# Kernel optimization log

Measured on AMD Instinct MI355X. Metric: run time of the kernel, lower is better.

## Reference

```python
import jax, jax.numpy as jnp
import numpy as np

B, L, SIZE, HEADS, AH, NBR, KER, DEPTH = 64, 512, 128, 8, 16, 15, 16, 3
MAXD = 20.0
N = B * L
EDGE = KER + 3 + 9 + 1  # 29


def _normalize(v):
    return v / (jnp.linalg.norm(v, axis=-1, keepdims=True) + 1e-8)


def _frames(pos):
    # local orientation frame per residue from consecutive CA displacements
    u = _normalize(pos[1:] - pos[:-1])            # (N-1,3)
    up = jnp.concatenate([u[:1], u], axis=0)      # u_{i-1}
    un = jnp.concatenate([u, u[-1:]], axis=0)     # u_i
    b = _normalize(up - un)
    n = _normalize(jnp.cross(up, un))
    return jnp.stack([b, n, jnp.cross(b, n)], axis=-1)  # (N,3,3)


def setup_inputs() -> dict:
    key = jax.random.key(0)
    ks = jax.random.split(key, 16)
    g = lambda i, shape, s=1.0: jax.random.normal(ks[i], shape, jnp.float32) * s
    return {
        "tertiary": g(0, (N, 3, 3), 10.0),
        "sequence": g(1, (N, 20)),
        "subgraph_indices": jnp.arange(N, dtype=jnp.int32) // L,
        "knn_noise": g(2, (B, L, L)),
        "embed_w": g(3, (27, SIZE), 0.1), "embed_b": jnp.zeros((SIZE,), jnp.float32),
        "wq": g(4, (DEPTH, SIZE, HEADS * AH), 0.08),
        "wk": g(5, (DEPTH, SIZE + EDGE, HEADS * AH), 0.08),
        "wv": g(6, (DEPTH, SIZE + EDGE, HEADS * AH), 0.08),
        "wo": g(7, (DEPTH, HEADS * AH, SIZE), 0.08),
        "mlp_w1": g(8, (DEPTH, SIZE, SIZE), 0.08), "mlp_b1": jnp.zeros((DEPTH, SIZE), jnp.float32),
        "mlp_w2": g(9, (DEPTH, SIZE, SIZE), 0.08), "mlp_b2": jnp.zeros((DEPTH, SIZE), jnp.float32),
        "mlp_w3": g(10, (DEPTH, SIZE, SIZE), 0.08), "mlp_b3": jnp.zeros((DEPTH, SIZE), jnp.float32),
        "pool_w": g(11, (4, SIZE, SIZE, 3), 0.05), "pool_b": jnp.zeros((4, SIZE), jnp.float32),
        "energy_w": g(12, (SIZE, 1), 0.1), "energy_b": jnp.zeros((1,), jnp.float32),
    }


def _forward(tertiary, sequence, knn_noise, embed_w, embed_b, wq, wk, wv, wo,
             mlp_w1, mlp_b1, mlp_w2, mlp_b2, mlp_w3, mlp_b3,
             pool_w, pool_b, energy_w, energy_b):
    pos = tertiary[:, 1]                                   # (N,3) CA positions
    R = _frames(pos)                                       # (N,3,3)
    # ---- kNN per contiguous protein group with noisy distances ----
    pg = pos.reshape(B, L, 3)
    dist = jnp.linalg.norm(pg[:, :, None] - pg[:, None, :], axis=-1)  # (B,L,L)
    closeness = -dist + 3.0 * knn_noise
    idx = jax.lax.top_k(closeness, NBR)[1]                 # (B,L,NBR) local
    nbr = (idx + (jnp.arange(B) * L)[:, None, None]).reshape(N, NBR)
    # ---- RBF relative encoding (RelativeStructure.message) ----
    dvec = pos[nbr] - pos[:, None]                         # (N,NBR,3)
    d = jnp.linalg.norm(dvec, axis=-1)                     # (N,NBR)
    mu = jnp.linspace(0.0, MAXD, KER)
    sigma = MAXD / KER
    rbf = jnp.exp(-(((d[..., None] - mu) / sigma) ** 2))   # (N,NBR,KER)
    dirs = jnp.einsum('nrc,nkr->nkc', R, dvec / (d[..., None] + 1e-8))
    relrot = jnp.einsum('nrc,nkrd->nkcd', R, R[nbr]).reshape(N, NBR, 9)
    ind = jnp.arange(N, dtype=tertiary.dtype)
    relind = (ind[nbr] - ind[:, None])[..., None]
    edge = jnp.concatenate([rbf, dirs, relrot, relind], axis=-1)  # (N,NBR,EDGE)
    # ---- structured graph-attention encoder ----
    h = jnp.ones((N, 27), tertiary.dtype) @ embed_w + embed_b
    inv_sqrt = 1.0 / np.sqrt(AH).astype(np.float32)
    for l in range(DEPTH):
        q = (h @ wq[l]).reshape(N, HEADS, AH)
        kv = jnp.concatenate([h[nbr], edge], axis=-1)      # (N,NBR,SIZE+EDGE)
        k = (kv @ wk[l]).reshape(N, NBR, HEADS, AH)
        v = (kv @ wv[l]).reshape(N, NBR, HEADS, AH)
        logits = jnp.einsum('nhd,nkhd->nhk', q, k) * inv_sqrt
        a = jax.nn.softmax(logits, axis=-1)
        o = jnp.einsum('nhk,nkhd->nhd', a, v).reshape(N, HEADS * AH) @ wo[l]
        h = h + o
        m = jax.nn.relu(h @ mlp_w1[l] + mlp_b1[l])
        m = jax.nn.relu(m @ mlp_w2[l] + mlp_b2[l])
        h = h + m @ mlp_w3[l] + mlp_b3[l]
    # ---- scatter-pad pool: residual conv + maxpool(2), x4, then length-sum ----
    x = h.reshape(B, L, SIZE).transpose(0, 2, 1)           # (B,SIZE,L)
    for i in range(4):
        y = jax.lax.conv_general_dilated(
            x, pool_w[i], (1,), ((1, 1),),
            dimension_numbers=('NCH', 'OIH', 'NCH')) + pool_b[i][None, :, None]
        x = x + jax.nn.leaky_relu(y, 0.01)
        Lc = x.shape[-1]
        x = x.reshape(B, SIZE, Lc // 2, 2).max(axis=-1)
    pooled = x.sum(axis=-1)                                # (B,SIZE)
    return pooled @ energy_w + energy_b                    # (B,1)


def reference(tertiary, sequence, subgraph_indices, knn_noise, embed_w, embed_b,
              wq, wk, wv, wo, mlp_w1, mlp_b1, mlp_w2, mlp_b2, mlp_w3, mlp_b3,
              pool_w, pool_b, energy_w, energy_b):
    # subgraph_indices encodes contiguous equal-size groups (arange // L)
    return _forward(tertiary, sequence, knn_noise, embed_w, embed_b, wq, wk, wv, wo,
                    mlp_w1, mlp_b1, mlp_w2, mlp_b2, mlp_w3, mlp_b3,
                    pool_w, pool_b, energy_w, energy_b)
```

## Files before the change

kernel.cpp:

```cpp
#include <hip/hip_runtime.h>
#include <math.h>

#define N_TOT 32768
#define NNBR 15
#define APW 8
#define ELPH 40
#define ETP 20
#define PLP 20

#define KNB 4096
#define FRB 128
#define PRB 3392

typedef __attribute__((ext_vector_type(8))) _Float16 f16x8;
typedef __attribute__((ext_vector_type(2))) _Float16 f16x2;
typedef __attribute__((ext_vector_type(4))) float f32x4;

#define CBAR() __asm__ volatile("" ::: "memory")
#define PAIR(v, c) __builtin_shufflevector(v, v, 2 * (c), 2 * (c) + 1)

__device__ __forceinline__ _Float16 f2h(float x) { return (_Float16)x; }

__device__ __forceinline__ float fdot2(f16x2 a, f16x2 b, float c) {
  float d;
  asm("v_dot2_f32_f16 %0, %1, %2, %3" : "=v"(d) : "v"(a), "v"(b), "v"(c));
  return d;
}

template <int CTRL>
__device__ __forceinline__ float dpp_mov_f32(float x) {
  return __int_as_float(
      __builtin_amdgcn_update_dpp(0, __float_as_int(x), CTRL, 0xf, 0xf, true));
}

template <int CTRL>
__device__ __forceinline__ unsigned dpp_max_u32(unsigned x) {
  unsigned y = (unsigned)__builtin_amdgcn_update_dpp(0, (int)x, CTRL, 0xf, 0xf, true);
  return y > x ? y : x;
}

template <int CTRL>
__device__ __forceinline__ unsigned long long dpp_max_u64(unsigned long long x) {
  unsigned lo = (unsigned)__builtin_amdgcn_update_dpp(
      0, (int)(unsigned)x, CTRL, 0xf, 0xf, true);
  unsigned hi = (unsigned)__builtin_amdgcn_update_dpp(
      0, (int)(unsigned)(x >> 32), CTRL, 0xf, 0xf, true);
  unsigned long long y = ((unsigned long long)hi << 32) | lo;
  return y > x ? y : x;
}

__device__ __forceinline__ void ins3v(unsigned s, int j,
                                      unsigned& m1v, int& i1,
                                      unsigned& m2v, int& i2,
                                      unsigned& m3v, int& i3) {
  bool g1 = s > m1v;
  unsigned t = g1 ? m1v : s;  int it = g1 ? i1 : j;
  m1v = g1 ? s : m1v;         i1  = g1 ? j  : i1;
  bool g2 = t > m2v;
  unsigned u = g2 ? m2v : t;  int iu = g2 ? i2 : it;
  m2v = g2 ? t : m2v;         i2  = g2 ? it : i2;
  bool g3 = u > m3v;
  m3v = g3 ? u : m3v;         i3  = g3 ? iu : i3;
}

__global__ __launch_bounds__(256) void k_pre(
    const float* __restrict__ tert, const float* __restrict__ noise,
    int* __restrict__ nbr, float* __restrict__ pos, float* __restrict__ R,
    const float* __restrict__ wq, const float* __restrict__ wk,
    const float* __restrict__ wv, const float* __restrict__ wo,
    const float* __restrict__ w1, const float* __restrict__ w2,
    const float* __restrict__ w3, _Float16* __restrict__ wbt,
    _Float16* __restrict__ wqk, _Float16* __restrict__ wpe,
    const float* __restrict__ pw, _Float16* __restrict__ wct,
    const float* __restrict__ ew, const float* __restrict__ ebias,
    _Float16* __restrict__ h) {
  __shared__ float posL[512 * 3];
  __shared__ float hvS[128];
  int bb = blockIdx.x, tid = threadIdx.x;
  if (bb < KNB) {
    int b = bb >> 6;
    int n0 = b << 9;
    for (int i = tid; i < 1536; i += 256) {
      int r = i / 3, c = i - r * 3;
      posL[i] = tert[(size_t)(n0 + r) * 9 + 3 + c];
    }
    __syncthreads();
    int wave = tid >> 6, lane = tid & 63;
    int l = lane & 31;
    int rloc = (bb & 63) * 8 + wave * 2 + (lane >> 5);
    int row = n0 + rloc;
    const float* nrow = noise + (size_t)row * 512;
    float pix = posL[rloc * 3 + 0];
    float piy = posL[rloc * 3 + 1];
    float piz = posL[rloc * 3 + 2];
    unsigned m1v = 0u, m2v = 0u, m3v = 0u;
    int i1 = 0, i2 = 0, i3 = 0;
#pragma unroll
    for (int jj = 0; jj < 16; jj++) {
      int j = l + jj * 32;
      float dx = posL[j * 3 + 0] - pix;
      float dy = posL[j * 3 + 1] - piy;
      float dz = posL[j * 3 + 2] - piz;
      float c = -sqrtf(dx * dx + dy * dy + dz * dz) + 3.f * nrow[j];
      unsigned u = __float_as_uint(c);
      unsigned s = u ^ (unsigned)(((int)u >> 31) | (int)0x80000000);
      ins3v(s, j, m1v, i1, m2v, i2, m3v, i3);
    }
    int jmine = 0;
#pragma unroll 1
    for (int it = 0; it < NNBR; it++) {
      unsigned r = m1v;
      r = dpp_max_u32<0x111>(r);
      r = dpp_max_u32<0x112>(r);
      r = dpp_max_u32<0x114>(r);
      r = dpp_max_u32<0x118>(r);
      r = dpp_max_u32<0x142>(r);
      unsigned gA = (unsigned)__builtin_amdgcn_readlane((int)r, 31);
      unsigned gB = (unsigned)__builtin_amdgcn_readlane((int)r, 63);
      unsigned gsel = (lane & 32) ? gB : gA;
      bool match = (m1v == gsel);
      unsigned long long mk = __ballot((int)match);
      unsigned mA = (unsigned)mk, mB = (unsigned)(mk >> 32);
      int jA = __builtin_amdgcn_readlane(i1, __ffs(mA) - 1);
      int jB = __builtin_amdgcn_readlane(i1, 31 + __ffs(mB));
      if (__popc(mA) > 1 || __popc(mB) > 1) {
        unsigned long long pk = ((unsigned long long)m1v << 9) | (unsigned)(511 - i1);
        pk = dpp_max_u64<0x111>(pk);
        pk = dpp_max_u64<0x112>(pk);
        pk = dpp_max_u64<0x114>(pk);
        pk = dpp_max_u64<0x118>(pk);
        pk = dpp_max_u64<0x142>(pk);
        unsigned pA = (unsigned)__builtin_amdgcn_readlane((int)(unsigned)pk, 31);
        unsigned pB = (unsigned)__builtin_amdgcn_readlane((int)(unsigned)pk, 63);
        if (__popc(mA) > 1) jA = 511 - (int)(pA & 511u);
        if (__popc(mB) > 1) jB = 511 - (int)(pB & 511u);
      }
      int j = (lane & 32) ? jB : jA;
      if (l == it) jmine = j;
      bool win = match && (i1 == j);
      if (win) { m1v = m2v; i1 = i2; m2v = m3v; i2 = i3; m3v = 0u; }
      if (__any((int)(win && m1v == 0u))) {
        if (win && m1v == 0u) {
          unsigned gv = gsel; int gj = j;
          unsigned a1 = 0u, a2 = 0u, a3 = 0u;
          int b1i = 0, b2i = 0, b3i = 0;
#pragma unroll 1
          for (int jj = 0; jj < 16; jj++) {
            int j2 = l + jj * 32;
            float dx = posL[j2 * 3 + 0] - pix;
            float dy = posL[j2 * 3 + 1] - piy;
            float dz = posL[j2 * 3 + 2] - piz;
            float c = -sqrtf(dx * dx + dy * dy + dz * dz) + 3.f * nrow[j2];
            unsigned u = __float_as_uint(c);
            unsigned s = u ^ (unsigned)(((int)u >> 31) | (int)0x80000000);
            bool keep = (s < gv) || (s == gv && j2 > gj);
            ins3v(keep ? s : 0u, j2, a1, b1i, a2, b2i, a3, b3i);
          }
          m1v = a1; i1 = b1i; m2v = a2; i2 = b2i; m3v = a3; i3 = b3i;
        }
      }
    }
    if (l < NNBR) nbr[(size_t)row * NNBR + l] = n0 + jmine;
  } else if (bb < KNB + FRB) {
    int n = (bb - KNB) * 256 + tid;
    if (n >= N_TOT) return;
    float px = tert[n * 9 + 3], py = tert[n * 9 + 4], pz = tert[n * 9 + 5];
    pos[n * 3 + 0] = px; pos[n * 3 + 1] = py; pos[n * 3 + 2] = pz;
    int i0 = (n > 0) ? (n - 1) : 0;
    int i1 = (n < N_TOT - 1) ? n : (N_TOT - 2);
    float ax = tert[(i0 + 1) * 9 + 3] - tert[i0 * 9 + 3];
    float ay = tert[(i0 + 1) * 9 + 4] - tert[i0 * 9 + 4];
    float az = tert[(i0 + 1) * 9 + 5] - tert[i0 * 9 + 5];
    float il = 1.f / (sqrtf(ax * ax + ay * ay + az * az) + 1e-8f);
    float ux = ax * il, uy = ay * il, uz = az * il;
    float cx = tert[(i1 + 1) * 9 + 3] - tert[i1 * 9 + 3];
    float cy = tert[(i1 + 1) * 9 + 4] - tert[i1 * 9 + 4];
    float cz = tert[(i1 + 1) * 9 + 5] - tert[i1 * 9 + 5];
    il = 1.f / (sqrtf(cx * cx + cy * cy + cz * cz) + 1e-8f);
    float vx = cx * il, vy = cy * il, vz = cz * il;
    float bx = ux - vx, by = uy - vy, bz = uz - vz;
    il = 1.f / (sqrtf(bx * bx + by * by + bz * bz) + 1e-8f);
    bx *= il; by *= il; bz *= il;
    float nx = uy * vz - uz * vy;
    float ny = uz * vx - ux * vz;
    float nz = ux * vy - uy * vx;
    il = 1.f / (sqrtf(nx * nx + ny * ny + nz * nz) + 1e-8f);
    nx *= il; ny *= il; nz *= il;
    float ex = by * nz - bz * ny;
    float ey = bz * nx - bx * nz;
    float ez = bx * ny - by * nx;
    float* Rn = R + (size_t)n * 9;
    Rn[0] = bx; Rn[1] = nx; Rn[2] = ex;
    Rn[3] = by; Rn[4] = ny; Rn[5] = ey;
    Rn[6] = bz; Rn[7] = nz; Rn[8] = ez;
  } else {
    int pb2 = bb - (KNB + FRB);
    if (pb2 < 1344) {
      int idx = pb2 * 256 + tid;
      int lL = idx / (7 * 16384);
      int r = idx % (7 * 16384);
      int w = r / 16384;
      int e = r % 16384;
      int k = e >> 7, n = e & 127;
      float val;
      switch (w) {
        case 0: val = wq[(size_t)lL * 16384 + e]; break;
        case 1: val = wk[(size_t)lL * 157 * 128 + e]; break;
        case 2: val = wv[(size_t)lL * 157 * 128 + e]; break;
        case 3: val = wo[(size_t)lL * 16384 + e]; break;
        case 4: val = w1[(size_t)lL * 16384 + e]; break;
        case 5: val = w2[(size_t)lL * 16384 + e]; break;
        default: val = w3[(size_t)lL * 16384 + e]; break;
      }
      wbt[(size_t)(lL * 7 + w) * 16384 + n * 128 + k] = f2h(val);
    } else if (pb2 < 1728) {
      int idx = (pb2 - 1344) * 256 + tid;
      int lL = idx / 32768;
      int r = idx % 32768;
      int blk = r >> 14;
      int jp = (r >> 7) & 127;
      int c = r & 127;
      int j = blk * 128 + jp;
      int hh = j >> 5, e = j & 31;
      float val = 0.f;
      if (e < 29) {
        const float* wqp = wq + (size_t)lL * 16384 + (size_t)c * 128 + hh * 16;
        const float* wkp = wk + (size_t)lL * 157 * 128 + (size_t)(128 + e) * 128 + hh * 16;
        float s = 0.f;
#pragma unroll
        for (int d = 0; d < 16; d++) s = fmaf(wqp[d], wkp[d], s);
        val = 0.25f * s;
      }
      wqk[(size_t)idx] = f2h(val);
    } else if (pb2 < 2112) {
      int idx = (pb2 - 1728) * 256 + tid;
      int lL = idx / 32768;
      int r = idx % 32768;
      int blk = r >> 14;
      int cout = (r >> 7) & 127;
      int jp = r & 127;
      int j = blk * 128 + jp;
      float val = 0.f;
      if (j < 232) {
        int e = j >> 3, hh = j & 7;
        const float* wvp = wv + (size_t)lL * 157 * 128 + (size_t)(128 + e) * 128 + hh * 16;
        const float* wop = wo + (size_t)lL * 16384 + (size_t)(hh * 16) * 128 + cout;
#pragma unroll
        for (int d = 0; d < 16; d++) val = fmaf(wvp[d], wop[d * 128], val);
      }
      wpe[(size_t)idx] = f2h(val);
    } else if (pb2 < 2880) {
      int idx = (pb2 - 2112) * 256 + tid;
      int kt = idx % 3;
      int rest = idx / 3;
      int i = rest % 128; rest /= 128;
      int oo = rest % 128;
      int s = rest / 128;
      wct[(((size_t)s * 3 + kt) * 128 + oo) * 128 + i] = f2h(pw[idx]);
    } else {
      int vb = pb2 - 2880;
      if (tid < 128) {
        float s = ebias[tid];
#pragma unroll
        for (int i = 0; i < 27; i++) s += ew[i * 128 + tid];
        hvS[tid] = s;
      }
      __syncthreads();
      size_t total = (size_t)N_TOT * 128;
      for (size_t j = (size_t)vb * 256 + tid; j < total; j += (size_t)512 * 256)
        h[j] = f2h(hvS[j & 127]);
    }
  }
}

__global__ __launch_bounds__(256) void k_edge(const float* __restrict__ pos,
                                              const float* __restrict__ R,
                                              const int* __restrict__ nbr,
                                              _Float16* __restrict__ edge) {
  int idx = blockIdx.x * 256 + threadIdx.x;
  if (idx >= N_TOT * NNBR) return;
  int n = idx / NNBR;
  int m = nbr[idx];
  float dx = pos[m * 3 + 0] - pos[n * 3 + 0];
  float dy = pos[m * 3 + 1] - pos[n * 3 + 1];
  float dz = pos[m * 3 + 2] - pos[n * 3 + 2];
  float d = sqrtf(dx * dx + dy * dy + dz * dz);
  _Float16 eb[32];
#pragma unroll
  for (int j = 0; j < 16; j++) {
    float mu = (20.f / 15.f) * (float)j;
    float t = (d - mu) * 0.8f;
    eb[j] = f2h(__expf(-t * t));
  }
  float inv = 1.f / (d + 1e-8f);
  float ux = dx * inv, uy = dy * inv, uz = dz * inv;
  float Rn[9], Rm[9];
#pragma unroll
  for (int j = 0; j < 9; j++) { Rn[j] = R[(size_t)n * 9 + j]; Rm[j] = R[(size_t)m * 9 + j]; }
#pragma unroll
  for (int cc = 0; cc < 3; cc++)
    eb[16 + cc] = f2h(Rn[0 * 3 + cc] * ux + Rn[1 * 3 + cc] * uy + Rn[2 * 3 + cc] * uz);
#pragma unroll
  for (int cc = 0; cc < 3; cc++)
#pragma unroll
    for (int dd = 0; dd < 3; dd++)
      eb[19 + cc * 3 + dd] = f2h(Rn[0 * 3 + cc] * Rm[0 * 3 + dd] +
                                 Rn[1 * 3 + cc] * Rm[1 * 3 + dd] +
                                 Rn[2 * 3 + cc] * Rm[2 * 3 + dd]);
  eb[28] = f2h((float)(m - n));
  eb[29] = (_Float16)0.f; eb[30] = (_Float16)0.f; eb[31] = (_Float16)0.f;
  _Float16* e = edge + (size_t)idx * 32;
#pragma unroll
  for (int v = 0; v < 4; v++)
    *(uint4*)(e + v * 8) = *(const uint4*)(&eb[v * 8]);
}

template <int NTHR>
__device__ __forceinline__ void stage_w_async(const _Float16* __restrict__ W,
                                              _Float16* Ws, int tid) {
  int wv = tid >> 6, lane = tid & 63;
  constexpr int ITERS = 16384 / (NTHR * 8);
#pragma unroll
  for (int it = 0; it < ITERS; it++) {
    int base = it * (NTHR * 8) + wv * 512;
    int off = base + lane * 8;
    int row = off >> 7;
    int cL = (off >> 3) & 15;
    int cS = cL ^ (row & 7);
    const _Float16* src = W + ((size_t)row << 7) + (cS << 3);
    __builtin_amdgcn_global_load_lds(
        (const __attribute__((address_space(1))) void*)src,
        (__attribute__((address_space(3))) void*)(Ws + base), 16, 0, 0);
  }
}
template <int NTHR, int ROWS>
__device__ __forceinline__ void stage_x(const _Float16* __restrict__ src, _Float16* X,
                                        int tid, int rowstride) {
  for (int j = tid; j < ROWS * 16; j += NTHR) {
    int row = j >> 4, seg = (j & 15) * 8;
    *(uint4*)&X[row * 136 + seg] = *(const uint4*)(src + (size_t)row * rowstride + seg);
  }
}
template <bool RESET>
__device__ __forceinline__ void gemm_tile_t(const _Float16* X, const _Float16* Ws,
                                            int wrow, int l16, int quad, f32x4 acc[8]) {
  if (RESET) {
#pragma unroll
    for (int t = 0; t < 8; t++) acc[t] = (f32x4){0.f, 0.f, 0.f, 0.f};
  }
#pragma unroll
  for (int kk = 0; kk < 4; kk++) {
    f16x8 a = *(const f16x8*)&X[(wrow + l16) * 136 + kk * 32 + quad * 8];
#pragma unroll
    for (int t = 0; t < 8; t++) {
      int rw = t * 16 + l16;
      f16x8 b = *(const f16x8*)&Ws[(rw << 7) + ((((kk << 2) + quad) ^ (rw & 7)) << 3)];
      acc[t] = __builtin_amdgcn_mfma_f32_16x16x32_f16(a, b, acc[t], 0, 0, 0);
    }
  }
}

__global__ __launch_bounds__(512) void k_qkv(const _Float16* __restrict__ A,
                                             const _Float16* __restrict__ Wqt,
                                             const _Float16* __restrict__ Wkt,
                                             const _Float16* __restrict__ Wvt,
                                             const _Float16* __restrict__ Wqk0,
                                             const _Float16* __restrict__ Wqk1,
                                             _Float16* __restrict__ q, _Float16* __restrict__ hk,
                                             _Float16* __restrict__ hv, _Float16* __restrict__ qkw) {
  __shared__ _Float16 X[128 * 136];
  __shared__ _Float16 Ws[128 * 128];
  int tid = threadIdx.x, r0 = blockIdx.x * 128;
  int lane = tid & 63, quad = lane >> 4, l16 = lane & 15, wrow = (tid >> 6) * 16;
  stage_x<512, 128>(A + (size_t)r0 * 128, X, tid, 128);
  const _Float16* wts[5] = {Wqt, Wkt, Wvt, Wqk0, Wqk1};
  f32x4 acc[8];
  for (int w = 0; w < 5; w++) {
    __syncthreads();
    stage_w_async<512>(wts[w], Ws, tid);
    __syncthreads();
    gemm_tile_t<true>(X, Ws, wrow, l16, quad, acc);
#pragma unroll
    for (int t = 0; t < 8; t++) {
      int col = t * 16 + l16;
#pragma unroll
      for (int r = 0; r < 4; r++) {
        float v = acc[t][r];
        int rowg = r0 + wrow + quad * 4 + r;
        if (w < 3) {
          _Float16* C = (w == 0) ? q : (w == 1) ? hk : hv;
          C[(size_t)rowg * 128 + col] = f2h(v);
        } else {
          qkw[(size_t)rowg * 256 + (w - 3) * 128 + col] = f2h(v);
        }
      }
    }
  }
}

__global__ __launch_bounds__(512) void k_post(const _Float16* __restrict__ o,
                                              const _Float16* __restrict__ pe_g,
                                              _Float16* __restrict__ h,
                                              const _Float16* __restrict__ Wot,
                                              const _Float16* __restrict__ Wpe0,
                                              const _Float16* __restrict__ Wpe1,
                                              const _Float16* __restrict__ W1t, const float* __restrict__ B1,
                                              const _Float16* __restrict__ W2t, const float* __restrict__ B2,
                                              const _Float16* __restrict__ W3t, const float* __restrict__ B3,
                                              const _Float16* __restrict__ Wqt,
                                              const _Float16* __restrict__ Wkt,
                                              const _Float16* __restrict__ Wvt,
                                              const _Float16* __restrict__ Wqk0,
                                              const _Float16* __restrict__ Wqk1,
                                              _Float16* __restrict__ qo, _Float16* __restrict__ hko,
                                              _Float16* __restrict__ hvo, _Float16* __restrict__ qkwo,
                                              int do_qkv) {
  __shared__ _Float16 X[128 * 136];
  __shared__ _Float16 Ws[128 * 128];
  int tid = threadIdx.x, r0 = blockIdx.x * 128;
  int lane = tid & 63, quad = lane >> 4, l16 = lane & 15, wrow = (tid >> 6) * 16;
  f32x4 acc[8], hres[8];
  stage_x<512, 128>(o + (size_t)r0 * 128, X, tid, 128);
  stage_w_async<512>(Wot, Ws, tid);
  __syncthreads();
  gemm_tile_t<true>(X, Ws, wrow, l16, quad, acc);
  const _Float16* wpes[2] = {Wpe0, Wpe1};
#pragma unroll 1
  for (int blk = 0; blk < 2; blk++) {
    __syncthreads();
    stage_x<512, 128>(pe_g + (size_t)r0 * 256 + blk * 128, X, tid, 256);
    stage_w_async<512>(wpes[blk], Ws, tid);
    __syncthreads();
    gemm_tile_t<false>(X, Ws, wrow, l16, quad, acc);
  }
#pragma unroll
  for (int t = 0; t < 8; t++) {
    int col = t * 16 + l16;
#pragma unroll
    for (int r = 0; r < 4; r++)
      hres[t][r] = acc[t][r] + (float)h[(size_t)(r0 + wrow + quad * 4 + r) * 128 + col];
  }
  __syncthreads();
#pragma unroll
  for (int t = 0; t < 8; t++) {
    int col = t * 16 + l16;
#pragma unroll
    for (int r = 0; r < 4; r++)
      X[(wrow + quad * 4 + r) * 136 + col] = f2h(hres[t][r]);
  }
  stage_w_async<512>(W1t, Ws, tid);
  __syncthreads();
  gemm_tile_t<true>(X, Ws, wrow, l16, quad, acc);
  __syncthreads();
#pragma unroll
  for (int t = 0; t < 8; t++) {
    int col = t * 16 + l16; float bv = B1[col];
#pragma unroll
    for (int r = 0; r < 4; r++)
      X[(wrow + quad * 4 + r) * 136 + col] = f2h(fmaxf(acc[t][r] + bv, 0.f));
  }
  stage_w_async<512>(W2t, Ws, tid);
  __syncthreads();
  gemm_tile_t<true>(X, Ws, wrow, l16, quad, acc);
  __syncthreads();
#pragma unroll
  for (int t = 0; t < 8; t++) {
    int col = t * 16 + l16; float bv = B2[col];
#pragma unroll
    for (int r = 0; r < 4; r++)
      X[(wrow + quad * 4 + r) * 136 + col] = f2h(fmaxf(acc[t][r] + bv, 0.f));
  }
  stage_w_async<512>(W3t, Ws, tid);
  __syncthreads();
  gemm_tile_t<true>(X, Ws, wrow, l16, quad, acc);
  __syncthreads();
#pragma unroll
  for (int t = 0; t < 8; t++) {
    int col = t * 16 + l16; float bv = B3[col];
#pragma unroll
    for (int r = 0; r < 4; r++) {
      float v = hres[t][r] + acc[t][r] + bv;
      h[(size_t)(r0 + wrow + quad * 4 + r) * 128 + col] = f2h(v);
      if (do_qkv) X[(wrow + quad * 4 + r) * 136 + col] = f2h(v);
    }
  }
  if (!do_qkv) return;
  const _Float16* wts[5] = {Wqt, Wkt, Wvt, Wqk0, Wqk1};
  for (int w = 0; w < 5; w++) {
    __syncthreads();
    stage_w_async<512>(wts[w], Ws, tid);
    __syncthreads();
    gemm_tile_t<true>(X, Ws, wrow, l16, quad, acc);
#pragma unroll
    for (int t = 0; t < 8; t++) {
      int col = t * 16 + l16;
#pragma unroll
      for (int r = 0; r < 4; r++) {
        float v = acc[t][r];
        int rowg = r0 + wrow + quad * 4 + r;
        if (w < 3) {
          _Float16* C = (w == 0) ? qo : (w == 1) ? hko : hvo;
          C[(size_t)rowg * 128 + col] = f2h(v);
        } else {
          qkwo[(size_t)rowg * 256 + (w - 3) * 128 + col] = f2h(v);
        }
      }
    }
  }
}

__global__ __launch_bounds__(256) void k_attn(const _Float16* __restrict__ q,
                                              const _Float16* __restrict__ hk,
                                              const _Float16* __restrict__ hv,
                                              const int* __restrict__ nbr,
                                              const _Float16* __restrict__ edge,
                                              const _Float16* __restrict__ qkw,
                                              _Float16* __restrict__ o,
                                              _Float16* __restrict__ pe_g) {
  __shared__ _Float16 elL[4][15 * ELPH];
  __shared__ float etL[4][32 * ETP];
  __shared__ float plL[4][8 * PLP];
  __shared__ int nbL[4][16];
  int tid = threadIdx.x, wave = tid >> 6, lane = tid & 63;
  _Float16* el = elL[wave]; float* et = etL[wave]; float* pl = plL[wave];
  int* nbl = nbL[wave];
  int h8 = lane & 7, k2 = lane >> 3, c2 = lane * 2, h5 = lane >> 3;
  int kst = lane >> 2, gst = lane & 3;
  if (lane < 32) et[lane * ETP + 15] = 0.f;
  int n0 = (blockIdx.x * 4 + wave) * APW;
#pragma unroll 1
  for (int ni = 0; ni < APW; ni++) {
    int n = n0 + ni;
    if (lane < 60) {
      f16x8 ev = *(const f16x8*)(edge + ((size_t)n * 15 + kst) * 32 + gst * 8);
      *(f16x8*)&el[kst * ELPH + gst * 8] = ev;
      int ebs = gst * 8;
      et[(ebs + 0) * ETP + kst] = (float)ev[0];
      et[(ebs + 1) * ETP + kst] = (float)ev[1];
      et[(ebs + 2) * ETP + kst] = (float)ev[2];
      et[(ebs + 3) * ETP + kst] = (float)ev[3];
      et[(ebs + 4) * ETP + kst] = (float)ev[4];
      et[(ebs + 5) * ETP + kst] = (float)ev[5];
      et[(ebs + 6) * ETP + kst] = (float)ev[6];
      et[(ebs + 7) * ETP + kst] = (float)ev[7];
    }
    if (lane < 15) nbl[lane] = nbr[(size_t)n * NNBR + lane];
    const _Float16* qs = qkw + (size_t)n * 256 + h8 * 32;
    f16x8 w0 = *(const f16x8*)qs, w1 = *(const f16x8*)(qs + 8);
    f16x8 w2 = *(const f16x8*)(qs + 16), w3 = *(const f16x8*)(qs + 24);
    const _Float16* qp = q + (size_t)n * 128 + h8 * 16;
    f16x8 qa = *(const f16x8*)qp, qb = *(const f16x8*)(qp + 8);
    CBAR();
#pragma unroll
    for (int p = 0; p < 2; p++) {
      int k = k2 + p * 8;
      if (k < 15) {
        int m = nbl[k];
        const _Float16* hkp = hk + (size_t)m * 128 + h8 * 16;
        f16x8 ha = *(const f16x8*)hkp, hb = *(const f16x8*)(hkp + 8);
        float d0 = 0.f, d1 = 0.f;
        d0 = fdot2(PAIR(qa, 0), PAIR(ha, 0), d0);
        d1 = fdot2(PAIR(qa, 1), PAIR(ha, 1), d1);
        d0 = fdot2(PAIR(qa, 2), PAIR(ha, 2), d0);
        d1 = fdot2(PAIR(qa, 3), PAIR(ha, 3), d1);
        d0 = fdot2(PAIR(qb, 0), PAIR(hb, 0), d0);
        d1 = fdot2(PAIR(qb, 1), PAIR(hb, 1), d1);
        d0 = fdot2(PAIR(qb, 2), PAIR(hb, 2), d0);
        d1 = fdot2(PAIR(qb, 3), PAIR(hb, 3), d1);
        f16x8 l0 = *(const f16x8*)&el[k * ELPH + 0];
        f16x8 l1 = *(const f16x8*)&el[k * ELPH + 8];
        f16x8 l2 = *(const f16x8*)&el[k * ELPH + 16];
        f16x8 l3 = *(const f16x8*)&el[k * ELPH + 24];
        float e0 = 0.f, e1 = 0.f;
        e0 = fdot2(PAIR(l0, 0), PAIR(w0, 0), e0);
        e1 = fdot2(PAIR(l0, 1), PAIR(w0, 1), e1);
        e0 = fdot2(PAIR(l0, 2), PAIR(w0, 2), e0);
        e1 = fdot2(PAIR(l0, 3), PAIR(w0, 3), e1);
        e0 = fdot2(PAIR(l1, 0), PAIR(w1, 0), e0);
        e1 = fdot2(PAIR(l1, 1), PAIR(w1, 1), e1);
        e0 = fdot2(PAIR(l1, 2), PAIR(w1, 2), e0);
        e1 = fdot2(PAIR(l1, 3), PAIR(w1, 3), e1);
        e0 = fdot2(PAIR(l2, 0), PAIR(w2, 0), e0);
        e1 = fdot2(PAIR(l2, 1), PAIR(w2, 1), e1);
        e0 = fdot2(PAIR(l2, 2), PAIR(w2, 2), e0);
        e1 = fdot2(PAIR(l2, 3), PAIR(w2, 3), e1);
        e0 = fdot2(PAIR(l3, 0), PAIR(w3, 0), e0);
        e1 = fdot2(PAIR(l3, 1), PAIR(w3, 1), e1);
        e0 = fdot2(PAIR(l3, 2), PAIR(w3, 2), e0);
        e1 = fdot2(PAIR(l3, 3), PAIR(w3, 3), e1);
        pl[h8 * PLP + k] = fmaf(0.25f, d0 + d1, e0 + e1);
      } else {
        pl[h8 * PLP + 15] = -1e30f;
      }
    }
    CBAR();
    {
      int hh = lane >> 3, g = lane & 7;
      float va = pl[hh * PLP + g];
      float vb = pl[hh * PLP + 8 + g];
      float mx = fmaxf(va, vb);
      mx = fmaxf(mx, dpp_mov_f32<0xB1>(mx));
      mx = fmaxf(mx, dpp_mov_f32<0x4E>(mx));
      mx = fmaxf(mx, dpp_mov_f32<0x141>(mx));
      float ea = __expf(va - mx), eb = __expf(vb - mx);
      float s = ea + eb;
      s += dpp_mov_f32<0xB1>(s);
      s += dpp_mov_f32<0x4E>(s);
      s += dpp_mov_f32<0x141>(s);
      float inv = 1.f / s;
      pl[hh * PLP + g] = ea * inv;
      pl[hh * PLP + 8 + g] = eb * inv;
    }
    CBAR();
    _Float16* peo = pe_g + (size_t)n * 256;
#pragma unroll
    for (int p = 0; p < 4; p++) {
      int j = p * 64 + lane;
      float s = 0.f;
      if (j < 232) {
        int e = j >> 3, hh = j & 7;
        f32x4 p0 = *(const f32x4*)&pl[hh * PLP + 0];
        f32x4 p1 = *(const f32x4*)&pl[hh * PLP + 4];
        f32x4 p2 = *(const f32x4*)&pl[hh * PLP + 8];
        f32x4 p3 = *(const f32x4*)&pl[hh * PLP + 12];
        f32x4 t0 = *(const f32x4*)&et[e * ETP + 0];
        f32x4 t1 = *(const f32x4*)&et[e * ETP + 4];
        f32x4 t2 = *(const f32x4*)&et[e * ETP + 8];
        f32x4 t3 = *(const f32x4*)&et[e * ETP + 12];
        s = p0[0]*t0[0] + p0[1]*t0[1] + p0[2]*t0[2] + p0[3]*t0[3]
          + p1[0]*t1[0] + p1[1]*t1[1] + p1[2]*t1[2] + p1[3]*t1[3]
          + p2[0]*t2[0] + p2[1]*t2[1] + p2[2]*t2[2] + p2[3]*t2[3]
          + p3[0]*t3[0] + p3[1]*t3[1] + p3[2]*t3[2] + p3[3]*t3[3];
      }
      peo[j] = f2h(s);
    }
    float pk[16];
    *(f32x4*)&pk[0]  = *(const f32x4*)&pl[h5 * PLP + 0];
    *(f32x4*)&pk[4]  = *(const f32x4*)&pl[h5 * PLP + 4];
    *(f32x4*)&pk[8]  = *(const f32x4*)&pl[h5 * PLP + 8];
    *(f32x4*)&pk[12] = *(const f32x4*)&pl[h5 * PLP + 12];
    float ox = 0.f, oy = 0.f;
#pragma unroll
    for (int k = 0; k < 15; k++) {
      int m = nbl[k];
      f16x2 hh = *(const f16x2*)(hv + (size_t)m * 128 + c2);
      ox = fmaf(pk[k], (float)hh[0], ox);
      oy = fmaf(pk[k], (float)hh[1], oy);
    }
    *(f16x2*)(o + (size_t)n * 128 + c2) = (f16x2){f2h(ox), f2h(oy)};
    CBAR();
  }
}

__global__ __launch_bounds__(256) void k_convpool_m(const _Float16* __restrict__ x,
                                                    const _Float16* __restrict__ Wc,
                                                    const float* __restrict__ bias,
                                                    _Float16* __restrict__ outp, int Tin) {
  __shared__ _Float16 Xs[66 * 136];
  __shared__ _Float16 Ws[128 * 128];
  int tid = threadIdx.x;
  int b = blockIdx.y;
  int t0 = blockIdx.x * 64;
  for (int j = tid; j < 66 * 16; j += 256) {
    int row = j >> 4, seg = (j & 15) * 8;
    int t = t0 - 1 + row;
    uint4 v = {0u, 0u, 0u, 0u};
    if (t >= 0 && t < Tin) v = *(const uint4*)(x + ((size_t)b * Tin + t) * 128 + seg);
    *(uint4*)&Xs[row * 136 + seg] = v;
  }
  int lane = tid & 63, quad = lane >> 4, l16 = lane & 15, wrow = (tid >> 6) * 16;
  f32x4 acc[8];
#pragma unroll
  for (int t = 0; t < 8; t++) acc[t] = (f32x4){0.f, 0.f, 0.f, 0.f};
  for (int kt = 0; kt < 3; kt++) {
    __syncthreads();
    stage_w_async<256>(Wc + (size_t)kt * 16384, Ws, tid);
    __syncthreads();
#pragma unroll
    for (int kk = 0; kk < 4; kk++) {
      f16x8 a = *(const f16x8*)&Xs[(wrow + l16 + kt) * 136 + kk * 32 + quad * 8];
#pragma unroll
      for (int t = 0; t < 8; t++) {
        int rw = t * 16 + l16;
        f16x8 bfr = *(const f16x8*)&Ws[(rw << 7) + ((((kk << 2) + quad) ^ (rw & 7)) << 3)];
        acc[t] = __builtin_amdgcn_mfma_f32_16x16x32_f16(a, bfr, acc[t], 0, 0, 0);
      }
    }
  }
  int Tout = Tin >> 1;
#pragma unroll
  for (int t = 0; t < 8; t++) {
    int col = t * 16 + l16;
    float bv = bias[col];
#pragma unroll
    for (int rp = 0; rp < 2; rp++) {
      int rl0 = wrow + quad * 4 + rp * 2;
      float y0 = acc[t][rp * 2] + bv;
      float y1 = acc[t][rp * 2 + 1] + bv;
      float z0 = (float)Xs[(rl0 + 1) * 136 + col] + (y0 >= 0.f ? y0 : 0.01f * y0);
      float z1 = (float)Xs[(rl0 + 2) * 136 + col] + (y1 >= 0.f ? y1 : 0.01f * y1);
      outp[((size_t)b * Tout + ((t0 + rl0) >> 1)) * 128 + col] = f2h(fmaxf(z0, z1));
    }
  }
}

__global__ __launch_bounds__(128) void k_final(const _Float16* __restrict__ x,
                                               const float* __restrict__ ew,
                                               const float* __restrict__ ebb,
                                               float* __restrict__ outp) {
  int b = blockIdx.x, cc = threadIdx.x;
  float s = 0.f;
#pragma unroll
  for (int t = 0; t < 32; t++) s += (float)x[((size_t)b * 32 + t) * 128 + cc];
  float v = s * ew[cc];
#pragma unroll
  for (int m = 1; m < 64; m <<= 1) v += __shfl_xor(v, m);
  __shared__ float red[2];
  if ((cc & 63) == 0) red[cc >> 6] = v;
  __syncthreads();
  if (cc == 0) outp[b] = red[0] + red[1] + ebb[0];
}

extern "C" void kernel_launch(void* const* d_in, const int* in_sizes, int n_in,
                              void* d_out, int out_size, void* d_ws, size_t ws_size,
                              hipStream_t stream) {
  (void)in_sizes; (void)n_in; (void)out_size; (void)ws_size;
  const float* tert    = (const float*)d_in[0];
  const float* noise   = (const float*)d_in[3];
  const float* embed_w = (const float*)d_in[4];
  const float* embed_b = (const float*)d_in[5];
  const float* wq = (const float*)d_in[6];
  const float* wk = (const float*)d_in[7];
  const float* wv = (const float*)d_in[8];
  const float* wo = (const float*)d_in[9];
  const float* w1 = (const float*)d_in[10];
  const float* b1 = (const float*)d_in[11];
  const float* w2 = (const float*)d_in[12];
  const float* b2 = (const float*)d_in[13];
  const float* w3 = (const float*)d_in[14];
  const float* b3 = (const float*)d_in[15];
  const float* pw = (const float*)d_in[16];
  const float* pb = (const float*)d_in[17];
  const float* ew = (const float*)d_in[18];
  const float* eb = (const float*)d_in[19];
  float* outp = (float*)d_out;

  char* W = (char*)d_ws;
  float* pos  = (float*)W;        W += 393216;
  float* R    = (float*)W;        W += 1179648;
  int*   nbr  = (int*)W;          W += 1966080;
  _Float16* edge = (_Float16*)W;  W += 31457280;
  _Float16* h    = (_Float16*)W;  W += 8388608;
  _Float16* q    = (_Float16*)W;  W += 8388608;
  _Float16* hk   = (_Float16*)W;  W += 8388608;
  _Float16* hv   = (_Float16*)W;  W += 8388608;
  _Float16* o    = (_Float16*)W;  W += 8388608;
  _Float16* qkw_g = (_Float16*)W; W += 16777216;
  _Float16* pe_g  = (_Float16*)W; W += 16777216;
  _Float16* xa   = (_Float16*)W;  W += 4194304;
  _Float16* xb   = (_Float16*)W;  W += 2097152;
  _Float16* wbt  = (_Float16*)W;  W += 688128;
  _Float16* wqk  = (_Float16*)W;  W += 196608;
  _Float16* wpe  = (_Float16*)W;  W += 196608;
  _Float16* wct  = (_Float16*)W;  W += 393216;

  k_pre<<<KNB + FRB + PRB, 256, 0, stream>>>(tert, noise, nbr, pos, R,
                                             wq, wk, wv, wo, w1, w2, w3, wbt,
                                             wqk, wpe, pw, wct, embed_w, embed_b, h);
  k_edge<<<1920, 256, 0, stream>>>(pos, R, nbr, edge);

  const _Float16* wt[3][7];
  for (int l = 0; l < 3; l++)
    for (int w = 0; w < 7; w++) wt[l][w] = wbt + (size_t)(l * 7 + w) * 16384;
  const _Float16* wqk_l[3][2];
  const _Float16* wpe_l[3][2];
  for (int l = 0; l < 3; l++)
    for (int bk = 0; bk < 2; bk++) {
      wqk_l[l][bk] = wqk + (size_t)(l * 2 + bk) * 16384;
      wpe_l[l][bk] = wpe + (size_t)(l * 2 + bk) * 16384;
    }

  k_qkv<<<256, 512, 0, stream>>>(h, wt[0][0], wt[0][1], wt[0][2],
                                 wqk_l[0][0], wqk_l[0][1], q, hk, hv, qkw_g);
  for (int l = 0; l < 3; l++) {
    k_attn<<<1024, 256, 0, stream>>>(q, hk, hv, nbr, edge, qkw_g, o, pe_g);
    int nl = l + 1;
    int do_qkv = (nl < 3) ? 1 : 0;
    k_post<<<256, 512, 0, stream>>>(o, pe_g, h, wt[l][3],
                                    wpe_l[l][0], wpe_l[l][1],
                                    wt[l][4], b1 + l * 128,
                                    wt[l][5], b2 + l * 128,
                                    wt[l][6], b3 + l * 128,
                                    do_qkv ? wt[nl][0] : nullptr,
                                    do_qkv ? wt[nl][1] : nullptr,
                                    do_qkv ? wt[nl][2] : nullptr,
                                    do_qkv ? wqk_l[nl][0] : nullptr,
                                    do_qkv ? wqk_l[nl][1] : nullptr,
                                    q, hk, hv, qkw_g, do_qkv);
  }

  k_convpool_m<<<dim3(8, 64), 256, 0, stream>>>(h,  wct + 0 * 49152, pb + 0,   xa, 512);
  k_convpool_m<<<dim3(4, 64), 256, 0, stream>>>(xa, wct + 1 * 49152, pb + 128, xb, 256);
  k_convpool_m<<<dim3(2, 64), 256, 0, stream>>>(xb, wct + 2 * 49152, pb + 256, xa, 128);
  k_convpool_m<<<dim3(1, 64), 256, 0, stream>>>(xa, wct + 3 * 49152, pb + 384, xb, 64);
  k_final<<<64, 128, 0, stream>>>(xb, ew, eb, outp);
}
```

Baseline: 466.8 us.

## Fuse edge features with first QKV and merge conv-pool stages into one kernel

Edge feature computation and the first-layer QKV projection are merged into a single launch via block-index dispatch, with the QKV and post-attention tiles shrunk to 64 rows and 256 threads. The four conv+maxpool stages and the final energy reduction are combined into one kernel per protein that keeps intermediates in LDS. This removes several launches and global round-trips but runs the conv chain with only 64 large-LDS blocks working serially over tiles.

Result: slower. 498.8 us (+6.9%).

```diff
diff --git a/kernel.cpp b/kernel.cpp
--- a/kernel.cpp
+++ b/kernel.cpp
@@ -11,6 +11,8 @@
 #define KNB 4096
 #define FRB 128
 #define PRB 3392
+
+#define EB 1920
 
 typedef __attribute__((ext_vector_type(8))) _Float16 f16x8;
 typedef __attribute__((ext_vector_type(2))) _Float16 f16x2;
@@ -273,48 +275,6 @@
   }
 }
 
-__global__ __launch_bounds__(256) void k_edge(const float* __restrict__ pos,
-                                              const float* __restrict__ R,
-                                              const int* __restrict__ nbr,
-                                              _Float16* __restrict__ edge) {
-  int idx = blockIdx.x * 256 + threadIdx.x;
-  if (idx >= N_TOT * NNBR) return;
-  int n = idx / NNBR;
-  int m = nbr[idx];
-  float dx = pos[m * 3 + 0] - pos[n * 3 + 0];
-  float dy = pos[m * 3 + 1] - pos[n * 3 + 1];
-  float dz = pos[m * 3 + 2] - pos[n * 3 + 2];
-  float d = sqrtf(dx * dx + dy * dy + dz * dz);
-  _Float16 eb[32];
-#pragma unroll
-  for (int j = 0; j < 16; j++) {
-    float mu = (20.f / 15.f) * (float)j;
-    float t = (d - mu) * 0.8f;
-    eb[j] = f2h(__expf(-t * t));
-  }
-  float inv = 1.f / (d + 1e-8f);
-  float ux = dx * inv, uy = dy * inv, uz = dz * inv;
-  float Rn[9], Rm[9];
-#pragma unroll
-  for (int j = 0; j < 9; j++) { Rn[j] = R[(size_t)n * 9 + j]; Rm[j] = R[(size_t)m * 9 + j]; }
-#pragma unroll
-  for (int cc = 0; cc < 3; cc++)
-    eb[16 + cc] = f2h(Rn[0 * 3 + cc] * ux + Rn[1 * 3 + cc] * uy + Rn[2 * 3 + cc] * uz);
-#pragma unroll
-  for (int cc = 0; cc < 3; cc++)
-#pragma unroll
-    for (int dd = 0; dd < 3; dd++)
-      eb[19 + cc * 3 + dd] = f2h(Rn[0 * 3 + cc] * Rm[0 * 3 + dd] +
-                                 Rn[1 * 3 + cc] * Rm[1 * 3 + dd] +
-                                 Rn[2 * 3 + cc] * Rm[2 * 3 + dd]);
-  eb[28] = f2h((float)(m - n));
-  eb[29] = (_Float16)0.f; eb[30] = (_Float16)0.f; eb[31] = (_Float16)0.f;
-  _Float16* e = edge + (size_t)idx * 32;
-#pragma unroll
-  for (int v = 0; v < 4; v++)
-    *(uint4*)(e + v * 8) = *(const uint4*)(&eb[v * 8]);
-}
-
 template <int NTHR>
 __device__ __forceinline__ void stage_w_async(const _Float16* __restrict__ W,
                                               _Float16* Ws, int tid) {
@@ -360,45 +320,89 @@
   }
 }
 
-__global__ __launch_bounds__(512) void k_qkv(const _Float16* __restrict__ A,
-                                             const _Float16* __restrict__ Wqt,
-                                             const _Float16* __restrict__ Wkt,
-                                             const _Float16* __restrict__ Wvt,
-                                             const _Float16* __restrict__ Wqk0,
-                                             const _Float16* __restrict__ Wqk1,
-                                             _Float16* __restrict__ q, _Float16* __restrict__ hk,
-                                             _Float16* __restrict__ hv, _Float16* __restrict__ qkw) {
-  __shared__ _Float16 X[128 * 136];
+__global__ __launch_bounds__(256) void k_eq(const float* __restrict__ pos,
+                                            const float* __restrict__ R,
+                                            const int* __restrict__ nbr,
+                                            _Float16* __restrict__ edge,
+                                            const _Float16* __restrict__ A,
+                                            const _Float16* __restrict__ Wqt,
+                                            const _Float16* __restrict__ Wkt,
+                                            const _Float16* __restrict__ Wvt,
+                                            const _Float16* __restrict__ Wqk0,
+                                            const _Float16* __restrict__ Wqk1,
+                                            _Float16* __restrict__ q, _Float16* __restrict__ hk,
+                                            _Float16* __restrict__ hv, _Float16* __restrict__ qkw) {
+  __shared__ _Float16 X[64 * 136];
   __shared__ _Float16 Ws[128 * 128];
-  int tid = threadIdx.x, r0 = blockIdx.x * 128;
-  int lane = tid & 63, quad = lane >> 4, l16 = lane & 15, wrow = (tid >> 6) * 16;
-  stage_x<512, 128>(A + (size_t)r0 * 128, X, tid, 128);
-  const _Float16* wts[5] = {Wqt, Wkt, Wvt, Wqk0, Wqk1};
-  f32x4 acc[8];
-  for (int w = 0; w < 5; w++) {
-    __syncthreads();
-    stage_w_async<512>(wts[w], Ws, tid);
-    __syncthreads();
-    gemm_tile_t<true>(X, Ws, wrow, l16, quad, acc);
-#pragma unroll
-    for (int t = 0; t < 8; t++) {
-      int col = t * 16 + l16;
-#pragma unroll
-      for (int r = 0; r < 4; r++) {
-        float v = acc[t][r];
-        int rowg = r0 + wrow + quad * 4 + r;
-        if (w < 3) {
-          _Float16* C = (w == 0) ? q : (w == 1) ? hk : hv;
-          C[(size_t)rowg * 128 + col] = f2h(v);
-        } else {
-          qkw[(size_t)rowg * 256 + (w - 3) * 128 + col] = f2h(v);
+  int bb = blockIdx.x, tid = threadIdx.x;
+  if (bb < EB) {
+    int idx = bb * 256 + tid;
+    if (idx >= N_TOT * NNBR) return;
+    int n = idx / NNBR;
+    int m = nbr[idx];
+    float dx = pos[m * 3 + 0] - pos[n * 3 + 0];
+    float dy = pos[m * 3 + 1] - pos[n * 3 + 1];
+    float dz = pos[m * 3 + 2] - pos[n * 3 + 2];
+    float d = sqrtf(dx * dx + dy * dy + dz * dz);
+    _Float16 eb[32];
+#pragma unroll
+    for (int j = 0; j < 16; j++) {
+      float mu = (20.f / 15.f) * (float)j;
+      float t = (d - mu) * 0.8f;
+      eb[j] = f2h(__expf(-t * t));
+    }
+    float inv = 1.f / (d + 1e-8f);
+    float ux = dx * inv, uy = dy * inv, uz = dz * inv;
+    float Rn[9], Rm[9];
+#pragma unroll
+    for (int j = 0; j < 9; j++) { Rn[j] = R[(size_t)n * 9 + j]; Rm[j] = R[(size_t)m * 9 + j]; }
+#pragma unroll
+    for (int cc = 0; cc < 3; cc++)
+      eb[16 + cc] = f2h(Rn[0 * 3 + cc] * ux + Rn[1 * 3 + cc] * uy + Rn[2 * 3 + cc] * uz);
+#pragma unroll
+    for (int cc = 0; cc < 3; cc++)
+#pragma unroll
+      for (int dd = 0; dd < 3; dd++)
+        eb[19 + cc * 3 + dd] = f2h(Rn[0 * 3 + cc] * Rm[0 * 3 + dd] +
+                                   Rn[1 * 3 + cc] * Rm[1 * 3 + dd] +
+                                   Rn[2 * 3 + cc] * Rm[2 * 3 + dd]);
+    eb[28] = f2h((float)(m - n));
+    eb[29] = (_Float16)0.f; eb[30] = (_Float16)0.f; eb[31] = (_Float16)0.f;
+    _Float16* e = edge + (size_t)idx * 32;
+#pragma unroll
+    for (int v = 0; v < 4; v++)
+      *(uint4*)(e + v * 8) = *(const uint4*)(&eb[v * 8]);
+  } else {
+    int r0 = (bb - EB) * 64;
+    int lane = tid & 63, quad = lane >> 4, l16 = lane & 15, wrow = (tid >> 6) * 16;
+    stage_x<256, 64>(A + (size_t)r0 * 128, X, tid, 128);
+    const _Float16* wts[5] = {Wqt, Wkt, Wvt, Wqk0, Wqk1};
+    f32x4 acc[8];
+    for (int w = 0; w < 5; w++) {
+      __syncthreads();
+      stage_w_async<256>(wts[w], Ws, tid);
+      __syncthreads();
+      gemm_tile_t<true>(X, Ws, wrow, l16, quad, acc);
+#pragma unroll
+      for (int t = 0; t < 8; t++) {
+        int col = t * 16 + l16;
+#pragma unroll
+        for (int r = 0; r < 4; r++) {
+          float v = acc[t][r];
+          int rowg = r0 + wrow + quad * 4 + r;
+          if (w < 3) {
+            _Float16* C = (w == 0) ? q : (w == 1) ? hk : hv;
+            C[(size_t)rowg * 128 + col] = f2h(v);
+          } else {
+            qkw[(size_t)rowg * 256 + (w - 3) * 128 + col] = f2h(v);
+          }
         }
       }
     }
   }
 }
 
-__global__ __launch_bounds__(512) void k_post(const _Float16* __restrict__ o,
+__global__ __launch_bounds__(256) void k_post(const _Float16* __restrict__ o,
                                               const _Float16* __restrict__ pe_g,
                                               _Float16* __restrict__ h,
                                               const _Float16* __restrict__ Wot,
@@ -415,21 +419,21 @@
                                               _Float16* __restrict__ qo, _Float16* __restrict__ hko,
                                               _Float16* __restrict__ hvo, _Float16* __restrict__ qkwo,
                                               int do_qkv) {
-  __shared__ _Float16 X[128 * 136];
+  __shared__ _Float16 X[64 * 136];
   __shared__ _Float16 Ws[128 * 128];
-  int tid = threadIdx.x, r0 = blockIdx.x * 128;
+  int tid = threadIdx.x, r0 = blockIdx.x * 64;
   int lane = tid & 63, quad = lane >> 4, l16 = lane & 15, wrow = (tid >> 6) * 16;
   f32x4 acc[8], hres[8];
-  stage_x<512, 128>(o + (size_t)r0 * 128, X, tid, 128);
-  stage_w_async<512>(Wot, Ws, tid);
+  stage_x<256, 64>(o + (size_t)r0 * 128, X, tid, 128);
+  stage_w_async<256>(Wot, Ws, tid);
   __syncthreads();
   gemm_tile_t<true>(X, Ws, wrow, l16, quad, acc);
   const _Float16* wpes[2] = {Wpe0, Wpe1};
 #pragma unroll 1
   for (int blk = 0; blk < 2; blk++) {
     __syncthreads();
-    stage_x<512, 128>(pe_g + (size_t)r0 * 256 + blk * 128, X, tid, 256);
-    stage_w_async<512>(wpes[blk], Ws, tid);
+    stage_x<256, 64>(pe_g + (size_t)r0 * 256 + blk * 128, X, tid, 256);
+    stage_w_async<256>(wpes[blk], Ws, tid);
     __syncthreads();
     gemm_tile_t<false>(X, Ws, wrow, l16, quad, acc);
   }
@@ -448,7 +452,7 @@
     for (int r = 0; r < 4; r++)
       X[(wrow + quad * 4 + r) * 136 + col] = f2h(hres[t][r]);
   }
-  stage_w_async<512>(W1t, Ws, tid);
+  stage_w_async<256>(W1t, Ws, tid);
   __syncthreads();
   gemm_tile_t<true>(X, Ws, wrow, l16, quad, acc);
   __syncthreads();
@@ -459,7 +463,7 @@
     for (int r = 0; r < 4; r++)
       X[(wrow + quad * 4 + r) * 136 + col] = f2h(fmaxf(acc[t][r] + bv, 0.f));
   }
-  stage_w_async<512>(W2t, Ws, tid);
+  stage_w_async<256>(W2t, Ws, tid);
   __syncthreads();
   gemm_tile_t<true>(X, Ws, wrow, l16, quad, acc);
   __syncthreads();
@@ -470,7 +474,7 @@
     for (int r = 0; r < 4; r++)
       X[(wrow + quad * 4 + r) * 136 + col] = f2h(fmaxf(acc[t][r] + bv, 0.f));
   }
-  stage_w_async<512>(W3t, Ws, tid);
+  stage_w_async<256>(W3t, Ws, tid);
   __syncthreads();
   gemm_tile_t<true>(X, Ws, wrow, l16, quad, acc);
   __syncthreads();
@@ -488,7 +492,7 @@
   const _Float16* wts[5] = {Wqt, Wkt, Wvt, Wqk0, Wqk1};
   for (int w = 0; w < 5; w++) {
     __syncthreads();
-    stage_w_async<512>(wts[w], Ws, tid);
+    stage_w_async<256>(wts[w], Ws, tid);
     __syncthreads();
     gemm_tile_t<true>(X, Ws, wrow, l16, quad, acc);
 #pragma unroll
@@ -652,73 +656,99 @@
   }
 }
 
-__global__ __launch_bounds__(256) void k_convpool_m(const _Float16* __restrict__ x,
-                                                    const _Float16* __restrict__ Wc,
-                                                    const float* __restrict__ bias,
-                                                    _Float16* __restrict__ outp, int Tin) {
+__device__ __forceinline__ void conv_mfma(const _Float16* Xs, const _Float16* Ws,
+                                          int wrow, int l16, int quad, int kt,
+                                          f32x4 acc[8]) {
+#pragma unroll
+  for (int kk = 0; kk < 4; kk++) {
+    f16x8 a = *(const f16x8*)&Xs[(wrow + l16 + kt) * 136 + kk * 32 + quad * 8];
+#pragma unroll
+    for (int t = 0; t < 8; t++) {
+      int rw = t * 16 + l16;
+      f16x8 bfr = *(const f16x8*)&Ws[(rw << 7) + ((((kk << 2) + quad) ^ (rw & 7)) << 3)];
+      acc[t] = __builtin_amdgcn_mfma_f32_16x16x32_f16(a, bfr, acc[t], 0, 0, 0);
+    }
+  }
+}
+
+template <bool GIN>
+__device__ void conv_stage(const _Float16* __restrict__ gin, const _Float16* IN,
+                           _Float16* OUT, const _Float16* __restrict__ Wc,
+                           const float* __restrict__ bias, int Tin,
+                           _Float16* Xs, _Float16* Ws, int tid) {
+  int lane = tid & 63, quad = lane >> 4, l16 = lane & 15, wrow = (tid >> 6) * 16;
+  int ntile = Tin >> 6;
+  int Tout = Tin >> 1;
+  for (int tt = 0; tt < ntile; tt++) {
+    int t0 = tt * 64;
+    __syncthreads();
+    for (int j = tid; j < 66 * 16; j += 256) {
+      int row = j >> 4, seg = (j & 15) * 8;
+      int t = t0 - 1 + row;
+      uint4 v = {0u, 0u, 0u, 0u};
+      if (t >= 0 && t < Tin) {
+        if (GIN) v = *(const uint4*)(gin + (size_t)t * 128 + seg);
+        else     v = *(const uint4*)(IN + t * 128 + seg);
+      }
+      *(uint4*)&Xs[row * 136 + seg] = v;
+    }
+    f32x4 acc[8];
+#pragma unroll
+    for (int t = 0; t < 8; t++) acc[t] = (f32x4){0.f, 0.f, 0.f, 0.f};
+    for (int kt = 0; kt < 3; kt++) {
+      __syncthreads();
+      stage_w_async<256>(Wc + (size_t)kt * 16384, Ws, tid);
+      __syncthreads();
+      conv_mfma(Xs, Ws, wrow, l16, quad, kt, acc);
+    }
+#pragma unroll
+    for (int t = 0; t < 8; t++) {
+      int col = t * 16 + l16;
+      float bv = bias[col];
+#pragma unroll
+      for (int rp = 0; rp < 2; rp++) {
+        int rl0 = wrow + quad * 4 + rp * 2;
+        float y0 = acc[t][rp * 2] + bv;
+        float y1 = acc[t][rp * 2 + 1] + bv;
+        float z0 = (float)Xs[(rl0 + 1) * 136 + col] + (y0 >= 0.f ? y0 : 0.01f * y0);
+        float z1 = (float)Xs[(rl0 + 2) * 136 + col] + (y1 >= 0.f ? y1 : 0.01f * y1);
+        OUT[((t0 + rl0) >> 1) * 128 + col] = f2h(fmaxf(z0, z1));
+      }
+    }
+    (void)Tout;
+  }
+  __syncthreads();
+}
+
+__global__ __launch_bounds__(256) void k_convall(const _Float16* __restrict__ h,
+                                                 const _Float16* __restrict__ wct,
+                                                 const float* __restrict__ pb,
+                                                 const float* __restrict__ ew,
+                                                 const float* __restrict__ ebb,
+                                                 float* __restrict__ outp) {
+  __shared__ _Float16 bufA[256 * 128];
+  __shared__ _Float16 bufB[128 * 128];
+  __shared__ _Float16 Ws[128 * 128];
   __shared__ _Float16 Xs[66 * 136];
-  __shared__ _Float16 Ws[128 * 128];
-  int tid = threadIdx.x;
-  int b = blockIdx.y;
-  int t0 = blockIdx.x * 64;
-  for (int j = tid; j < 66 * 16; j += 256) {
-    int row = j >> 4, seg = (j & 15) * 8;
-    int t = t0 - 1 + row;
-    uint4 v = {0u, 0u, 0u, 0u};
-    if (t >= 0 && t < Tin) v = *(const uint4*)(x + ((size_t)b * Tin + t) * 128 + seg);
-    *(uint4*)&Xs[row * 136 + seg] = v;
-  }
-  int lane = tid & 63, quad = lane >> 4, l16 = lane & 15, wrow = (tid >> 6) * 16;
-  f32x4 acc[8];
-#pragma unroll
-  for (int t = 0; t < 8; t++) acc[t] = (f32x4){0.f, 0.f, 0.f, 0.f};
-  for (int kt = 0; kt < 3; kt++) {
-    __syncthreads();
-    stage_w_async<256>(Wc + (size_t)kt * 16384, Ws, tid);
-    __syncthreads();
-#pragma unroll
-    for (int kk = 0; kk < 4; kk++) {
-      f16x8 a = *(const f16x8*)&Xs[(wrow + l16 + kt) * 136 + kk * 32 + quad * 8];
-#pragma unroll
-      for (int t = 0; t < 8; t++) {
-        int rw = t * 16 + l16;
-        f16x8 bfr = *(const f16x8*)&Ws[(rw << 7) + ((((kk << 2) + quad) ^ (rw & 7)) << 3)];
-        acc[t] = __builtin_amdgcn_mfma_f32_16x16x32_f16(a, bfr, acc[t], 0, 0, 0);
-      }
-    }
-  }
-  int Tout = Tin >> 1;
-#pragma unroll
-  for (int t = 0; t < 8; t++) {
-    int col = t * 16 + l16;
-    float bv = bias[col];
-#pragma unroll
-    for (int rp = 0; rp < 2; rp++) {
-      int rl0 = wrow + quad * 4 + rp * 2;
-      float y0 = acc[t][rp * 2] + bv;
-      float y1 = acc[t][rp * 2 + 1] + bv;
-      float z0 = (float)Xs[(rl0 + 1) * 136 + col] + (y0 >= 0.f ? y0 : 0.01f * y0);
-      float z1 = (float)Xs[(rl0 + 2) * 136 + col] + (y1 >= 0.f ? y1 : 0.01f * y1);
-      outp[((size_t)b * Tout + ((t0 + rl0) >> 1)) * 128 + col] = f2h(fmaxf(z0, z1));
-    }
-  }
-}
-
-__global__ __launch_bounds__(128) void k_final(const _Float16* __restrict__ x,
-                                               const float* __restrict__ ew,
-                                               const float* __restrict__ ebb,
-                                               float* __restrict__ outp) {
-  int b = blockIdx.x, cc = threadIdx.x;
-  float s = 0.f;
-#pragma unroll
-  for (int t = 0; t < 32; t++) s += (float)x[((size_t)b * 32 + t) * 128 + cc];
-  float v = s * ew[cc];
+  __shared__ float red[2];
+  int b = blockIdx.x, tid = threadIdx.x;
+  const _Float16* gin = h + (size_t)(b * 512) * 128;
+  conv_stage<true >(gin, nullptr, bufA, wct + 0 * 49152, pb + 0,   512, Xs, Ws, tid);
+  conv_stage<false>(nullptr, bufA, bufB, wct + 1 * 49152, pb + 128, 256, Xs, Ws, tid);
+  conv_stage<false>(nullptr, bufB, bufA, wct + 2 * 49152, pb + 256, 128, Xs, Ws, tid);
+  conv_stage<false>(nullptr, bufA, bufB, wct + 3 * 49152, pb + 384,  64, Xs, Ws, tid);
+  float v = 0.f;
+  if (tid < 128) {
+    float s = 0.f;
+#pragma unroll
+    for (int t = 0; t < 32; t++) s += (float)bufB[t * 128 + tid];
+    v = s * ew[tid];
+  }
 #pragma unroll
   for (int m = 1; m < 64; m <<= 1) v += __shfl_xor(v, m);
-  __shared__ float red[2];
-  if ((cc & 63) == 0) red[cc >> 6] = v;
-  __syncthreads();
-  if (cc == 0) outp[b] = red[0] + red[1] + ebb[0];
+  if (tid < 128 && (tid & 63) == 0) red[tid >> 6] = v;
+  __syncthreads();
+  if (tid == 0) outp[b] = red[0] + red[1] + ebb[0];
 }
 
 extern "C" void kernel_launch(void* const* d_in, const int* in_sizes, int n_in,
@@ -763,11 +793,11 @@
   _Float16* wqk  = (_Float16*)W;  W += 196608;
   _Float16* wpe  = (_Float16*)W;  W += 196608;
   _Float16* wct  = (_Float16*)W;  W += 393216;
+  (void)xa; (void)xb;
 
   k_pre<<<KNB + FRB + PRB, 256, 0, stream>>>(tert, noise, nbr, pos, R,
                                              wq, wk, wv, wo, w1, w2, w3, wbt,
                                              wqk, wpe, pw, wct, embed_w, embed_b, h);
-  k_edge<<<1920, 256, 0, stream>>>(pos, R, nbr, edge);
 
   const _Float16* wt[3][7];
   for (int l = 0; l < 3; l++)
@@ -780,13 +810,14 @@
       wpe_l[l][bk] = wpe + (size_t)(l * 2 + bk) * 16384;
     }
 
-  k_qkv<<<256, 512, 0, stream>>>(h, wt[0][0], wt[0][1], wt[0][2],
-                                 wqk_l[0][0], wqk_l[0][1], q, hk, hv, qkw_g);
+  k_eq<<<EB + 512, 256, 0, stream>>>(pos, R, nbr, edge,
+                                     h, wt[0][0], wt[0][1], wt[0][2],
+                                     wqk_l[0][0], wqk_l[0][1], q, hk, hv, qkw_g);
   for (int l = 0; l < 3; l++) {
     k_attn<<<1024, 256, 0, stream>>>(q, hk, hv, nbr, edge, qkw_g, o, pe_g);
     int nl = l + 1;
     int do_qkv = (nl < 3) ? 1 : 0;
-    k_post<<<256, 512, 0, stream>>>(o, pe_g, h, wt[l][3],
+    k_post<<<512, 256, 0, stream>>>(o, pe_g, h, wt[l][3],
                                     wpe_l[l][0], wpe_l[l][1],
                                     wt[l][4], b1 + l * 128,
                                     wt[l][5], b2 + l * 128,
@@ -799,9 +830,5 @@
                                     q, hk, hv, qkw_g, do_qkv);
   }
 
-  k_convpool_m<<<dim3(8, 64), 256, 0, stream>>>(h,  wct + 0 * 49152, pb + 0,   xa, 512);
-  k_convpool_m<<<dim3(4, 64), 256, 0, stream>>>(xa, wct + 1 * 49152, pb + 128, xb, 256);
-  k_convpool_m<<<dim3(2, 64), 256, 0, stream>>>(xb, wct + 2 * 49152, pb + 256, xa, 128);
-  k_convpool_m<<<dim3(1, 64), 256, 0, stream>>>(xa, wct + 3 * 49152, pb + 384, xb, 64);
-  k_final<<<64, 128, 0, stream>>>(xb, ew, eb, outp);
-}
+  k_convall<<<64, 256, 0, stream>>>(h, wct, pb, ew, eb, outp);
+}
```
